# Optimization experiments

Hardware: AMD Instinct MI355X
Metric: run time of the kernel (lower is better)

Reference implementation:

```python
import jax, jax.numpy as jnp
import numpy as np

H = 8      # n_heads
DK = 64    # d_k per head
EPS = 1e-5       # InstanceNorm1d eps
SLOPE = 0.01     # LeakyReLU negative slope


def setup_inputs() -> dict:
    key = jax.random.key(0)
    ks = jax.random.split(key, 6)
    B, C, L = 16, 256, 1024
    HD = H * DK  # 512
    return {
        "x": jax.random.normal(ks[0], (B, C, L), dtype=jnp.float32),
        "Wq": jax.random.normal(ks[1], (HD, C), dtype=jnp.float32) * 0.02,
        "Wk": jax.random.normal(ks[2], (HD, C), dtype=jnp.float32) * 0.02,
        "Wv": jax.random.normal(ks[3], (HD, C), dtype=jnp.float32) * 0.02,
        "Wo": jax.random.normal(ks[4], (C, HD), dtype=jnp.float32) * 0.02,
        "gamma": jax.random.normal(ks[5], (1,), dtype=jnp.float32),
    }


def reference(x, Wq, Wk, Wv, Wo, gamma):
    B, C, L = x.shape
    # conv1x1 projections (bias=False) == channel matmuls -> [B, H*DK, L]
    # then reshape/permute into heads: [B, H, L, DK]
    def proj(W):
        y = jnp.einsum('oc,bcl->bol', W, x)          # [B, H*DK, L]
        return y.reshape(B, H, DK, L).transpose(0, 1, 3, 2)  # [B, H, L, DK]

    q, k, v = proj(Wq), proj(Wk), proj(Wv)
    # softmax-free linear attention: (Q K^T / d_k) V
    logits = jnp.einsum('bhld,bhmd->bhlm', q, k) / DK  # [B, H, L, L]
    out = jnp.einsum('bhlm,bhmd->bhld', logits, v)     # [B, H, L, DK]
    # merge heads back to channel-first [B, H*DK, L]
    merged = out.transpose(0, 1, 3, 2).reshape(B, H * DK, L)
    # output conv1x1 -> [B, C, L]
    o = jnp.einsum('oc,bcl->bol', Wo, merged)
    # InstanceNorm1d (affine=False): normalize over L per (b, c)
    mu = jnp.mean(o, axis=-1, keepdims=True)
    var = jnp.var(o, axis=-1, keepdims=True)
    o = (o - mu) * jax.lax.rsqrt(var + EPS)
    # gamma-scaled residual + LeakyReLU
    y = o * gamma + x
    return jnp.where(y >= 0, y, SLOPE * y)
```

## Files before the change

kernel.cpp:

```cpp
#include <hip/hip_runtime.h>

typedef __bf16 bf16;
typedef bf16 bf16x8 __attribute__((ext_vector_type(8)));
typedef bf16 bf16x4 __attribute__((ext_vector_type(4)));
typedef float f32x4 __attribute__((ext_vector_type(4)));

#define EPS 1e-5f
#define SLOPE 0.01f

__device__ __forceinline__ void gld_lds16(const bf16* g, bf16* l) {
    __builtin_amdgcn_global_load_lds(
        (const __attribute__((address_space(1))) unsigned int*)g,
        (__attribute__((address_space(3))) unsigned int*)l, 16, 0, 0);
}

__global__ __launch_bounds__(256) void prep_kernel(
    const float* __restrict__ x,
    const float* __restrict__ Wq, const float* __restrict__ Wk,
    const float* __restrict__ Wv, const float* __restrict__ Wo,
    bf16* __restrict__ xT, bf16* __restrict__ xB,
    bf16* __restrict__ WkB, bf16* __restrict__ WvB,
    bf16* __restrict__ WoB, bf16* __restrict__ WqT)
{
    __shared__ float tile[64][65];
    const int id = blockIdx.x;
    const int t = threadIdx.x;
    if (id < 1024) {
        const int lt = id & 15, ct = (id >> 4) & 3, b = id >> 6;
        {
            const int cl = t >> 2;
            const int l4 = (t & 3) << 4;
            const float* src = x + (size_t)(b * 256 + ct * 64 + cl) * 1024 + lt * 64 + l4;
            float4 v0 = ((const float4*)src)[0];
            float4 v1 = ((const float4*)src)[1];
            float4 v2 = ((const float4*)src)[2];
            float4 v3 = ((const float4*)src)[3];
            bf16x8 r0, r1;
            r0[0]=(bf16)v0.x; r0[1]=(bf16)v0.y; r0[2]=(bf16)v0.z; r0[3]=(bf16)v0.w;
            r0[4]=(bf16)v1.x; r0[5]=(bf16)v1.y; r0[6]=(bf16)v1.z; r0[7]=(bf16)v1.w;
            r1[0]=(bf16)v2.x; r1[1]=(bf16)v2.y; r1[2]=(bf16)v2.z; r1[3]=(bf16)v2.w;
            r1[4]=(bf16)v3.x; r1[5]=(bf16)v3.y; r1[6]=(bf16)v3.z; r1[7]=(bf16)v3.w;
            bf16* xbd = xB + (size_t)(b * 256 + ct * 64 + cl) * 1024 + lt * 64 + l4;
            *(bf16x8*)xbd = r0;
            *(bf16x8*)(xbd + 8) = r1;
            float* tr = &tile[cl][l4];
            tr[0]=v0.x; tr[1]=v0.y; tr[2]=v0.z; tr[3]=v0.w;
            tr[4]=v1.x; tr[5]=v1.y; tr[6]=v1.z; tr[7]=v1.w;
            tr[8]=v2.x; tr[9]=v2.y; tr[10]=v2.z; tr[11]=v2.w;
            tr[12]=v3.x; tr[13]=v3.y; tr[14]=v3.z; tr[15]=v3.w;
        }
        __syncthreads();
        {
            const int lw = t >> 2;
            const int ec = (t & 3) << 4;
            bf16x8 o0, o1;
            #pragma unroll
            for (int ii = 0; ii < 8; ++ii) {
                o0[ii] = (bf16)tile[ec + ii][lw];
                o1[ii] = (bf16)tile[ec + 8 + ii][lw];
            }
            bf16* dst = xT + (size_t)(b * 1024 + lt * 64 + lw) * 256 + ct * 64 + ec;
            *(bf16x8*)dst = o0;
            *(bf16x8*)(dst + 8) = o1;
        }
    } else if (id < 1408) {
        const int i = (id - 1024) * 1024 + t * 4;
        const float* src; bf16* dst;
        if (i < 131072)      { src = Wk + i;            dst = WkB + i; }
        else if (i < 262144) { src = Wv + (i - 131072); dst = WvB + (i - 131072); }
        else                 { src = Wo + (i - 262144); dst = WoB + (i - 262144); }
        float4 v = *(const float4*)src;
        bf16x4 o;
        o[0]=(bf16)v.x; o[1]=(bf16)v.y; o[2]=(bf16)v.z; o[3]=(bf16)v.w;
        *(bf16x4*)dst = o;
    } else {
        const int id2 = id - 1408;
        const int h = id2 >> 2, ct = id2 & 3;
        {
            const int e  = t >> 2;
            const int c4 = (t & 3) << 4;
            const float* src = Wq + (size_t)(h * 64 + e) * 256 + ct * 64 + c4;
            float4 v0 = ((const float4*)src)[0];
            float4 v1 = ((const float4*)src)[1];
            float4 v2 = ((const float4*)src)[2];
            float4 v3 = ((const float4*)src)[3];
            float* tr = &tile[e][c4];
            tr[0]=v0.x; tr[1]=v0.y; tr[2]=v0.z; tr[3]=v0.w;
            tr[4]=v1.x; tr[5]=v1.y; tr[6]=v1.z; tr[7]=v1.w;
            tr[8]=v2.x; tr[9]=v2.y; tr[10]=v2.z; tr[11]=v2.w;
            tr[12]=v3.x; tr[13]=v3.y; tr[14]=v3.z; tr[15]=v3.w;
        }
        __syncthreads();
        {
            const int c  = t >> 2;
            const int e4 = (t & 3) << 4;
            bf16x8 o0, o1;
            #pragma unroll
            for (int ii = 0; ii < 8; ++ii) {
                o0[ii] = (bf16)tile[e4 + ii][c];
                o1[ii] = (bf16)tile[e4 + 8 + ii][c];
            }
            bf16* dst = WqT + (size_t)h * 16384 + (size_t)(ct * 64 + c) * 64 + e4;
            *(bf16x8*)dst = o0;
            *(bf16x8*)(dst + 8) = o1;
        }
    }
}

template<int KDIM, typename OutT>
__global__ __launch_bounds__(256) void gemm128_bt(
    const bf16* __restrict__ A, const bf16* __restrict__ Bt, OutT* __restrict__ C,
    long long sA, long long sBt, long long sC, int ldC)
{
    __shared__ bf16 As[128 * 32];
    __shared__ bf16 Bs[128 * 32];
    const int z = blockIdx.z;
    A  += (size_t)z * sA;
    Bt += (size_t)z * sBt;
    C  += (size_t)z * sC;
    const int m0 = blockIdx.x * 128;
    const int n0 = blockIdx.y * 128;
    const int t = threadIdx.x, w = t >> 6, l = t & 63;
    const int srow = w * 16 + (l >> 2);
    const int ske  = (l & 3) * 8;
    const bf16* ga = A  + (size_t)(m0 + srow) * KDIM + ske;
    const bf16* gb = Bt + (size_t)(n0 + srow) * KDIM + ske;
    bf16* la = As + srow * 32 + ske;
    bf16* lb = Bs + srow * 32 + ske;
    const int lm = l & 15, lq = l >> 4;
    const int wm = (w & 1) * 64, wn = (w >> 1) * 64;

    f32x4 acc[4][4] = {};
    for (int kt = 0; kt < KDIM / 32; ++kt) {
        const int k0 = kt * 32;
        gld_lds16(ga + k0, la);
        gld_lds16(ga + k0 + (size_t)64 * KDIM, la + 64 * 32);
        gld_lds16(gb + k0, lb);
        gld_lds16(gb + k0 + (size_t)64 * KDIM, lb + 64 * 32);
        __syncthreads();
        bf16x8 af[4], bfr[4];
        #pragma unroll
        for (int i = 0; i < 4; ++i)
            af[i] = *(const bf16x8*)(As + (wm + i * 16 + lm) * 32 + lq * 8);
        #pragma unroll
        for (int j = 0; j < 4; ++j)
            bfr[j] = *(const bf16x8*)(Bs + (wn + j * 16 + lm) * 32 + lq * 8);
        #pragma unroll
        for (int i = 0; i < 4; ++i)
            #pragma unroll
            for (int j = 0; j < 4; ++j)
                acc[i][j] = __builtin_amdgcn_mfma_f32_16x16x32_bf16(af[i], bfr[j], acc[i][j], 0, 0, 0);
        __syncthreads();
    }
    #pragma unroll
    for (int i = 0; i < 4; ++i)
        #pragma unroll
        for (int j = 0; j < 4; ++j) {
            const int row = m0 + wm + i * 16 + lq * 4;
            const int col = n0 + wn + j * 16 + lm;
            OutT* cp = C + (size_t)row * ldC + col;
            #pragma unroll
            for (int r = 0; r < 4; ++r)
                cp[(size_t)r * ldC] = (OutT)acc[i][j][r];
        }
}

__global__ __launch_bounds__(256) void tm_kernel(
    const bf16* __restrict__ S, const bf16* __restrict__ WkB,
    const bf16* __restrict__ WqT, bf16* __restrict__ WmT)
{
    __shared__ __align__(16) bf16 regA[16384];
    __shared__ __align__(16) bf16 Qb[16384];
    bf16* Sc = regA;
    bf16* Kc = regA + 8192;
    bf16* Tb = regA;

    const int bh = blockIdx.x;
    const int b = bh >> 3, h = bh & 7;
    const bf16* Sg = S   + (size_t)b * 131072 + (size_t)h * 64 * 256;
    const bf16* Kg = WkB + (size_t)h * 64 * 256;
    const bf16* Qg = WqT + (size_t)h * 16384;
    const int t = threadIdx.x, w = t >> 6, l = t & 63;
    const int lm = l & 15, lq = l >> 4;

    #pragma unroll
    for (int it = 0; it < 8; ++it) {
        const int idx = it * 256 + t;
        const int r = idx >> 3, s = idx & 7;
        gld_lds16(Qg + (size_t)r * 64 + (s ^ (r & 7)) * 8, Qb + r * 64 + s * 8);
    }

    f32x4 accT[4] = {};
    for (int ck = 0; ck < 2; ++ck) {
        const int k0 = ck * 128;
        #pragma unroll
        for (int it = 0; it < 4; ++it) {
            const int idx = it * 256 + t;
            const int r = idx >> 4, s = idx & 15;
            const int gs = (s ^ (r & 7)) * 8;
            gld_lds16(Sg + (size_t)r * 256 + k0 + gs, Sc + r * 128 + s * 8);
            gld_lds16(Kg + (size_t)r * 256 + k0 + gs, Kc + r * 128 + s * 8);
        }
        __syncthreads();
        #pragma unroll
        for (int ks = 0; ks < 4; ++ks) {
            const int q = ks * 4 + lq;
            const int ra = w * 16 + lm;
            bf16x8 a = *(const bf16x8*)(Sc + ra * 128 + (q ^ (ra & 7)) * 8);
            #pragma unroll
            for (int nf = 0; nf < 4; ++nf) {
                const int rb = nf * 16 + lm;
                bf16x8 bb = *(const bf16x8*)(Kc + rb * 128 + (q ^ (rb & 7)) * 8);
                accT[nf] = __builtin_amdgcn_mfma_f32_16x16x32_bf16(a, bb, accT[nf], 0, 0, 0);
            }
        }
        __syncthreads();
    }
    #pragma unroll
    for (int nf = 0; nf < 4; ++nf)
        #pragma unroll
        for (int ri = 0; ri < 4; ++ri) {
            const int row = w * 16 + lq * 4 + ri;
            const int col = nf * 16 + lm;
            Tb[row * 64 + (((col >> 3) ^ (row & 7)) << 3) + (col & 7)] =
                (bf16)(accT[nf][ri] * 0.015625f);
        }
    __syncthreads();

    f32x4 accM[4][4] = {};
    #pragma unroll
    for (int ks = 0; ks < 2; ++ks) {
        const int q = ks * 4 + lq;
        bf16x8 bfrag[4];
        #pragma unroll
        for (int nf = 0; nf < 4; ++nf) {
            const int rb = nf * 16 + lm;
            bfrag[nf] = *(const bf16x8*)(Tb + rb * 64 + (q ^ (rb & 7)) * 8);
        }
        #pragma unroll
        for (int mf = 0; mf < 4; ++mf) {
            const int ra = w * 64 + mf * 16 + lm;
            bf16x8 a = *(const bf16x8*)(Qb + ra * 64 + (q ^ (ra & 7)) * 8);
            #pragma unroll
            for (int nf = 0; nf < 4; ++nf)
                accM[mf][nf] = __builtin_amdgcn_mfma_f32_16x16x32_bf16(a, bfrag[nf], accM[mf][nf], 0, 0, 0);
        }
    }
    bf16* Wg = WmT + (size_t)b * 131072 + h * 64;
    #pragma unroll
    for (int mf = 0; mf < 4; ++mf)
        #pragma unroll
        for (int nf = 0; nf < 4; ++nf)
            #pragma unroll
            for (int ri = 0; ri < 4; ++ri) {
                const int c = w * 64 + mf * 16 + lq * 4 + ri;
                const int d = nf * 16 + lm;
                Wg[(size_t)c * 512 + d] = (bf16)accM[mf][nf][ri];
            }
}

__global__ __launch_bounds__(256) void norm_kernel(
    const bf16* __restrict__ o, const bf16* __restrict__ xB,
    const float* __restrict__ gamma, float* __restrict__ y)
{
    const size_t row = blockIdx.x;
    const bf16* orow = o + row * 1024;
    const bf16* xrow = xB + row * 1024;
    float* yrow = y + row * 1024;
    const int tid = threadIdx.x;

    bf16x4 ov = *(const bf16x4*)(orow + tid * 4);
    float4 v = {(float)ov[0], (float)ov[1], (float)ov[2], (float)ov[3]};
    float s  = v.x + v.y + v.z + v.w;
    float ss = v.x * v.x + v.y * v.y + v.z * v.z + v.w * v.w;
    #pragma unroll
    for (int off = 32; off > 0; off >>= 1) {
        s  += __shfl_down(s, off);
        ss += __shfl_down(ss, off);
    }
    __shared__ float red[10];
    const int wave = tid >> 6, lane = tid & 63;
    if (lane == 0) { red[wave] = s; red[4 + wave] = ss; }
    __syncthreads();
    if (tid == 0) {
        float a  = red[0] + red[1] + red[2] + red[3];
        float b2 = red[4] + red[5] + red[6] + red[7];
        float mu = a * (1.0f / 1024.0f);
        float var = b2 * (1.0f / 1024.0f) - mu * mu;
        red[8] = mu;
        red[9] = rsqrtf(var + EPS);
    }
    __syncthreads();
    const float mu = red[8], inv = red[9], g = gamma[0];
    bf16x4 xv4 = *(const bf16x4*)(xrow + tid * 4);
    float4 r;
    r.x = (v.x - mu) * inv * g + (float)xv4[0];
    r.y = (v.y - mu) * inv * g + (float)xv4[1];
    r.z = (v.z - mu) * inv * g + (float)xv4[2];
    r.w = (v.w - mu) * inv * g + (float)xv4[3];
    r.x = r.x >= 0.f ? r.x : SLOPE * r.x;
    r.y = r.y >= 0.f ? r.y : SLOPE * r.y;
    r.z = r.z >= 0.f ? r.z : SLOPE * r.z;
    r.w = r.w >= 0.f ? r.w : SLOPE * r.w;
    ((float4*)yrow)[tid] = r;
}

extern "C" void kernel_launch(void* const* d_in, const int* in_sizes, int n_in,
                              void* d_out, int out_size, void* d_ws, size_t ws_size,
                              hipStream_t stream) {
    const float* x     = (const float*)d_in[0];
    const float* Wq    = (const float*)d_in[1];
    const float* Wk    = (const float*)d_in[2];
    const float* Wv    = (const float*)d_in[3];
    const float* Wo    = (const float*)d_in[4];
    const float* gamma = (const float*)d_in[5];
    float* y = (float*)d_out;

    char* wsb = (char*)d_ws;
    bf16* xT  = (bf16*)(wsb);
    bf16* xB  = (bf16*)(wsb +  8388608);
    bf16* WkB = (bf16*)(wsb + 16777216);
    bf16* WvB = (bf16*)(wsb + 17039360);
    bf16* WoB = (bf16*)(wsb + 17301504);
    bf16* WqT = (bf16*)(wsb + 17563648);
    bf16* G   = (bf16*)(wsb + 17825792);
    bf16* S   = (bf16*)(wsb + 19922944);
    bf16* WmT = (bf16*)(wsb + 24117248);
    bf16* Wt  = (bf16*)(wsb + 28311552);
    bf16* o   = (bf16*)(wsb + 30408704);

    prep_kernel<<<dim3(1440), 256, 0, stream>>>(x, Wq, Wk, Wv, Wo, xT, xB, WkB, WvB, WoB, WqT);

    gemm128_bt<1024, bf16><<<dim3(2, 2, 16), 256, 0, stream>>>(
        xB, xB, G, 262144LL, 262144LL, 65536LL, 256);

    gemm128_bt<256, bf16><<<dim3(4, 2, 16), 256, 0, stream>>>(
        WvB, G, S, 0LL, 65536LL, 131072LL, 256);

    tm_kernel<<<dim3(128), 256, 0, stream>>>(S, WkB, WqT, WmT);

    gemm128_bt<512, bf16><<<dim3(2, 2, 16), 256, 0, stream>>>(
        WoB, WmT, Wt, 0LL, 131072LL, 65536LL, 256);

    gemm128_bt<256, bf16><<<dim3(2, 8, 16), 256, 0, stream>>>(
        Wt, xT, o, 65536LL, 262144LL, 262144LL, 1024);

    norm_kernel<<<dim3(4096), 256, 0, stream>>>(o, xB, gamma, y);
}
```

Measured before the change: 139.0 us.

## Fuse projection chain into one kernel and fuse output GEMMs with instance norm

Merges the S = Wv·G GEMM into the per-head tm kernel, so S stays in LDS and is never written to or read back from global memory. Separately, it fuses the Wo·WmT GEMM, the final GEMM against x and the InstanceNorm/residual/LeakyReLU epilogue into one kernel per (batch, 16-channel tile). This removes the Wt and o intermediates and cuts the launch count from seven to four. The trade-off is fewer, heavier blocks (128 and 256) with large LDS footprints, which may underfill the GPU. The Wt product is also recomputed per channel tile rather than shared.

```diff
diff --git a/kernel.cpp b/kernel.cpp
--- a/kernel.cpp
+++ b/kernel.cpp
@@ -165,85 +165,151 @@
         }
 }
 
-__global__ __launch_bounds__(256) void tm_kernel(
-    const bf16* __restrict__ S, const bf16* __restrict__ WkB,
-    const bf16* __restrict__ WqT, bf16* __restrict__ WmT)
+__global__ __launch_bounds__(256) void chain_kernel(
+    const bf16* __restrict__ G, const bf16* __restrict__ WvB,
+    const bf16* __restrict__ WkB, const bf16* __restrict__ WqT,
+    bf16* __restrict__ WmT)
 {
-    __shared__ __align__(16) bf16 regA[16384];
-    __shared__ __align__(16) bf16 Qb[16384];
-    bf16* Sc = regA;
-    bf16* Kc = regA + 8192;
-    bf16* Tb = regA;
+    __shared__ __align__(16) bf16 bufA[64 * 256];
+    __shared__ __align__(16) bf16 bufB[256 * 64];
+    __shared__ __align__(16) bf16 Ss[64 * 256];
+    __shared__ __align__(16) bf16 Tb[64 * 64];
 
     const int bh = blockIdx.x;
     const int b = bh >> 3, h = bh & 7;
-    const bf16* Sg = S   + (size_t)b * 131072 + (size_t)h * 64 * 256;
-    const bf16* Kg = WkB + (size_t)h * 64 * 256;
-    const bf16* Qg = WqT + (size_t)h * 16384;
     const int t = threadIdx.x, w = t >> 6, l = t & 63;
     const int lm = l & 15, lq = l >> 4;
 
     #pragma unroll
     for (int it = 0; it < 8; ++it) {
-        const int idx = it * 256 + t;
-        const int r = idx >> 3, s = idx & 7;
-        gld_lds16(Qg + (size_t)r * 64 + (s ^ (r & 7)) * 8, Qb + r * 64 + s * 8);
-    }
-
-    f32x4 accT[4] = {};
-    for (int ck = 0; ck < 2; ++ck) {
-        const int k0 = ck * 128;
-        #pragma unroll
-        for (int it = 0; it < 4; ++it) {
-            const int idx = it * 256 + t;
-            const int r = idx >> 4, s = idx & 15;
-            const int gs = (s ^ (r & 7)) * 8;
-            gld_lds16(Sg + (size_t)r * 256 + k0 + gs, Sc + r * 128 + s * 8);
-            gld_lds16(Kg + (size_t)r * 256 + k0 + gs, Kc + r * 128 + s * 8);
-        }
-        __syncthreads();
-        #pragma unroll
-        for (int ks = 0; ks < 4; ++ks) {
-            const int q = ks * 4 + lq;
-            const int ra = w * 16 + lm;
-            bf16x8 a = *(const bf16x8*)(Sc + ra * 128 + (q ^ (ra & 7)) * 8);
+        const int slot = it * 256 + t;
+        const int d = slot >> 5, seg = slot & 31;
+        const int kq = (seg & 24) | ((seg & 7) ^ (d & 7));
+        gld_lds16(WvB + (size_t)(h * 64 + d) * 256 + kq * 8, bufA + slot * 8);
+    }
+    f32x4 accS[4][4] = {};
+    for (int ck = 0; ck < 4; ++ck) {
+        #pragma unroll
+        for (int it = 0; it < 8; ++it) {
+            const int slot = it * 256 + t;
+            const int cp = slot >> 3, seg = slot & 7;
+            const int kq = seg ^ (cp & 7);
+            gld_lds16(G + (size_t)b * 65536 + (size_t)cp * 256 + ck * 64 + kq * 8,
+                      bufB + slot * 8);
+        }
+        __syncthreads();
+        #pragma unroll
+        for (int kt = 0; kt < 2; ++kt) {
+            bf16x8 af[4], bfr[4];
+            #pragma unroll
+            for (int mf = 0; mf < 4; ++mf) {
+                const int m = mf * 16 + lm;
+                const int kqg = ck * 8 + kt * 4 + lq;
+                const int seg = (kqg & 24) | ((kqg & 7) ^ (m & 7));
+                af[mf] = *(const bf16x8*)(bufA + m * 256 + seg * 8);
+            }
             #pragma unroll
             for (int nf = 0; nf < 4; ++nf) {
-                const int rb = nf * 16 + lm;
-                bf16x8 bb = *(const bf16x8*)(Kc + rb * 128 + (q ^ (rb & 7)) * 8);
-                accT[nf] = __builtin_amdgcn_mfma_f32_16x16x32_bf16(a, bb, accT[nf], 0, 0, 0);
-            }
-        }
-        __syncthreads();
-    }
-    #pragma unroll
-    for (int nf = 0; nf < 4; ++nf)
-        #pragma unroll
-        for (int ri = 0; ri < 4; ++ri) {
-            const int row = w * 16 + lq * 4 + ri;
-            const int col = nf * 16 + lm;
-            Tb[row * 64 + (((col >> 3) ^ (row & 7)) << 3) + (col & 7)] =
-                (bf16)(accT[nf][ri] * 0.015625f);
-        }
+                const int n = w * 64 + nf * 16 + lm;
+                const int kq = kt * 4 + lq;
+                const int seg = kq ^ (n & 7);
+                bfr[nf] = *(const bf16x8*)(bufB + n * 64 + seg * 8);
+            }
+            #pragma unroll
+            for (int mf = 0; mf < 4; ++mf)
+                #pragma unroll
+                for (int nf = 0; nf < 4; ++nf)
+                    accS[mf][nf] = __builtin_amdgcn_mfma_f32_16x16x32_bf16(
+                        af[mf], bfr[nf], accS[mf][nf], 0, 0, 0);
+        }
+        __syncthreads();
+    }
+    #pragma unroll
+    for (int mf = 0; mf < 4; ++mf)
+        #pragma unroll
+        for (int nf = 0; nf < 4; ++nf)
+            #pragma unroll
+            for (int r = 0; r < 4; ++r) {
+                const int d = mf * 16 + lq * 4 + r;
+                const int cp = w * 64 + nf * 16 + lm;
+                const int s32 = cp >> 3;
+                const int s = (s32 & 24) | ((s32 & 7) ^ (d & 7));
+                Ss[d * 256 + s * 8 + (cp & 7)] = (bf16)accS[mf][nf][r];
+            }
+    #pragma unroll
+    for (int it = 0; it < 8; ++it) {
+        const int slot = it * 256 + t;
+        const int e = slot >> 5, seg = slot & 31;
+        const int kq = (seg & 24) | ((seg & 7) ^ (e & 7));
+        gld_lds16(WkB + (size_t)(h * 64 + e) * 256 + kq * 8, bufB + slot * 8);
+    }
     __syncthreads();
 
+    const int mh = (w & 1) * 32, nh = (w >> 1) * 32;
+    f32x4 accT[2][2] = {};
+    #pragma unroll
+    for (int kt = 0; kt < 8; ++kt) {
+        bf16x8 af[2], bfr[2];
+        #pragma unroll
+        for (int mf = 0; mf < 2; ++mf) {
+            const int m = mh + mf * 16 + lm;
+            const int kqg = kt * 4 + lq;
+            const int seg = (kqg & 24) | ((kqg & 7) ^ (m & 7));
+            af[mf] = *(const bf16x8*)(Ss + m * 256 + seg * 8);
+        }
+        #pragma unroll
+        for (int nf = 0; nf < 2; ++nf) {
+            const int n = nh + nf * 16 + lm;
+            const int kqg = kt * 4 + lq;
+            const int seg = (kqg & 24) | ((kqg & 7) ^ (n & 7));
+            bfr[nf] = *(const bf16x8*)(bufB + n * 256 + seg * 8);
+        }
+        #pragma unroll
+        for (int mf = 0; mf < 2; ++mf)
+            #pragma unroll
+            for (int nf = 0; nf < 2; ++nf)
+                accT[mf][nf] = __builtin_amdgcn_mfma_f32_16x16x32_bf16(
+                    af[mf], bfr[nf], accT[mf][nf], 0, 0, 0);
+    }
+    __syncthreads();
+    #pragma unroll
+    for (int mf = 0; mf < 2; ++mf)
+        #pragma unroll
+        for (int nf = 0; nf < 2; ++nf)
+            #pragma unroll
+            for (int r = 0; r < 4; ++r) {
+                const int d = mh + mf * 16 + lq * 4 + r;
+                const int e = nh + nf * 16 + lm;
+                const int seg = (e >> 3) ^ (d & 7);
+                Tb[d * 64 + seg * 8 + (e & 7)] = (bf16)(accT[mf][nf][r] * 0.015625f);
+            }
+    #pragma unroll
+    for (int it = 0; it < 8; ++it) {
+        const int slot = it * 256 + t;
+        const int c = slot >> 3, seg = slot & 7;
+        const int kq = seg ^ (c & 7);
+        gld_lds16(WqT + (size_t)h * 16384 + (size_t)c * 64 + kq * 8, bufA + slot * 8);
+    }
+    __syncthreads();
+
     f32x4 accM[4][4] = {};
     #pragma unroll
-    for (int ks = 0; ks < 2; ++ks) {
-        const int q = ks * 4 + lq;
-        bf16x8 bfrag[4];
+    for (int kt = 0; kt < 2; ++kt) {
+        const int kq = kt * 4 + lq;
+        bf16x8 bfr[4];
         #pragma unroll
         for (int nf = 0; nf < 4; ++nf) {
-            const int rb = nf * 16 + lm;
-            bfrag[nf] = *(const bf16x8*)(Tb + rb * 64 + (q ^ (rb & 7)) * 8);
+            const int n = nf * 16 + lm;
+            bfr[nf] = *(const bf16x8*)(Tb + n * 64 + (kq ^ (n & 7)) * 8);
         }
         #pragma unroll
         for (int mf = 0; mf < 4; ++mf) {
-            const int ra = w * 64 + mf * 16 + lm;
-            bf16x8 a = *(const bf16x8*)(Qb + ra * 64 + (q ^ (ra & 7)) * 8);
+            const int m = w * 64 + mf * 16 + lm;
+            bf16x8 a = *(const bf16x8*)(bufA + m * 64 + (kq ^ (m & 7)) * 8);
             #pragma unroll
             for (int nf = 0; nf < 4; ++nf)
-                accM[mf][nf] = __builtin_amdgcn_mfma_f32_16x16x32_bf16(a, bfrag[nf], accM[mf][nf], 0, 0, 0);
+                accM[mf][nf] = __builtin_amdgcn_mfma_f32_16x16x32_bf16(
+                    a, bfr[nf], accM[mf][nf], 0, 0, 0);
         }
     }
     bf16* Wg = WmT + (size_t)b * 131072 + h * 64;
@@ -252,57 +318,163 @@
         #pragma unroll
         for (int nf = 0; nf < 4; ++nf)
             #pragma unroll
-            for (int ri = 0; ri < 4; ++ri) {
-                const int c = w * 64 + mf * 16 + lq * 4 + ri;
+            for (int r = 0; r < 4; ++r) {
+                const int c = w * 64 + mf * 16 + lq * 4 + r;
                 const int d = nf * 16 + lm;
-                Wg[(size_t)c * 512 + d] = (bf16)accM[mf][nf][ri];
+                Wg[(size_t)c * 512 + d] = (bf16)accM[mf][nf][r];
             }
 }
 
-__global__ __launch_bounds__(256) void norm_kernel(
-    const bf16* __restrict__ o, const bf16* __restrict__ xB,
+__global__ __launch_bounds__(256) void outnorm_kernel(
+    const bf16* __restrict__ WoB, const bf16* __restrict__ WmT,
+    const bf16* __restrict__ xT, const bf16* __restrict__ xB,
     const float* __restrict__ gamma, float* __restrict__ y)
 {
-    const size_t row = blockIdx.x;
-    const bf16* orow = o + row * 1024;
-    const bf16* xrow = xB + row * 1024;
-    float* yrow = y + row * 1024;
-    const int tid = threadIdx.x;
-
-    bf16x4 ov = *(const bf16x4*)(orow + tid * 4);
-    float4 v = {(float)ov[0], (float)ov[1], (float)ov[2], (float)ov[3]};
-    float s  = v.x + v.y + v.z + v.w;
-    float ss = v.x * v.x + v.y * v.y + v.z * v.z + v.w * v.w;
-    #pragma unroll
-    for (int off = 32; off > 0; off >>= 1) {
-        s  += __shfl_down(s, off);
-        ss += __shfl_down(ss, off);
-    }
-    __shared__ float red[10];
-    const int wave = tid >> 6, lane = tid & 63;
-    if (lane == 0) { red[wave] = s; red[4 + wave] = ss; }
+    __shared__ __align__(16) bf16 chunkBuf[32768];
+    __shared__ __align__(16) bf16 WoS[16 * 512];
+    __shared__ __align__(16) bf16 WtS[16 * 256];
+    __shared__ float redS[4][16], redQ[4][16], bmu[16], binv[16];
+
+    const int b = blockIdx.x >> 4, ct = blockIdx.x & 15;
+    const int c0 = ct * 16;
+    const int t = threadIdx.x, w = t >> 6, l = t & 63;
+    const int lm = l & 15, lq = l >> 4;
+
+    #pragma unroll
+    for (int it = 0; it < 4; ++it) {
+        const int slot = it * 256 + t;
+        const int co = slot >> 6, seg = slot & 63;
+        const int kq = (seg & 56) | ((seg & 7) ^ (co & 7));
+        gld_lds16(WoB + (size_t)(c0 + co) * 512 + kq * 8, WoS + slot * 8);
+    }
+    f32x4 acc1[4] = {};
+    for (int ck = 0; ck < 8; ++ck) {
+        const int k0 = ck * 64;
+        #pragma unroll
+        for (int it = 0; it < 8; ++it) {
+            const int slot = it * 256 + t;
+            const int ci = slot >> 3, seg = slot & 7;
+            const int kq = seg ^ (ci & 7);
+            gld_lds16(WmT + (size_t)b * 131072 + (size_t)ci * 512 + k0 + kq * 8,
+                      chunkBuf + slot * 8);
+        }
+        __syncthreads();
+        #pragma unroll
+        for (int kt = 0; kt < 2; ++kt) {
+            const int kqg = ck * 8 + kt * 4 + lq;
+            const int sa = (kqg & 56) | ((kqg & 7) ^ (lm & 7));
+            bf16x8 a = *(const bf16x8*)(WoS + lm * 512 + sa * 8);
+            #pragma unroll
+            for (int nf = 0; nf < 4; ++nf) {
+                const int n = w * 64 + nf * 16 + lm;
+                const int kq = kt * 4 + lq;
+                bf16x8 bb = *(const bf16x8*)(chunkBuf + n * 64 + (kq ^ (n & 7)) * 8);
+                acc1[nf] = __builtin_amdgcn_mfma_f32_16x16x32_bf16(a, bb, acc1[nf], 0, 0, 0);
+            }
+        }
+        __syncthreads();
+    }
+    #pragma unroll
+    for (int nf = 0; nf < 4; ++nf)
+        #pragma unroll
+        for (int r = 0; r < 4; ++r) {
+            const int co = lq * 4 + r;
+            const int ci = w * 64 + nf * 16 + lm;
+            const int s32 = ci >> 3;
+            const int s = (s32 & 24) | ((s32 & 7) ^ (co & 7));
+            WtS[co * 256 + s * 8 + (ci & 7)] = (bf16)acc1[nf][r];
+        }
     __syncthreads();
-    if (tid == 0) {
-        float a  = red[0] + red[1] + red[2] + red[3];
-        float b2 = red[4] + red[5] + red[6] + red[7];
-        float mu = a * (1.0f / 1024.0f);
-        float var = b2 * (1.0f / 1024.0f) - mu * mu;
-        red[8] = mu;
-        red[9] = rsqrtf(var + EPS);
-    }
+
+    f32x4 acc2[16] = {};
+    for (int ck = 0; ck < 8; ++ck) {
+        const int k0 = ck * 32;
+        #pragma unroll
+        for (int it = 0; it < 16; ++it) {
+            const int slot = it * 256 + t;
+            const int ln = slot >> 2, seg = slot & 3;
+            const int kq = seg ^ (ln & 3);
+            gld_lds16(xT + (size_t)b * 262144 + (size_t)ln * 256 + k0 + kq * 8,
+                      chunkBuf + slot * 8);
+        }
+        __syncthreads();
+        const int kqg = ck * 4 + lq;
+        const int sa = (kqg & 24) | ((kqg & 7) ^ (lm & 7));
+        bf16x8 a = *(const bf16x8*)(WtS + lm * 256 + sa * 8);
+        #pragma unroll
+        for (int j = 0; j < 16; ++j) {
+            const int n = w * 256 + j * 16 + lm;
+            bf16x8 bb = *(const bf16x8*)(chunkBuf + n * 32 + ((lq ^ (n & 3)) * 8));
+            acc2[j] = __builtin_amdgcn_mfma_f32_16x16x32_bf16(a, bb, acc2[j], 0, 0, 0);
+        }
+        __syncthreads();
+    }
+
+    float s[4] = {}, q[4] = {};
+    #pragma unroll
+    for (int j = 0; j < 16; ++j)
+        #pragma unroll
+        for (int r = 0; r < 4; ++r) {
+            const float v = acc2[j][r];
+            s[r] += v; q[r] += v * v;
+        }
+    #pragma unroll
+    for (int off = 1; off < 16; off <<= 1)
+        #pragma unroll
+        for (int r = 0; r < 4; ++r) {
+            s[r] += __shfl_xor(s[r], off);
+            q[r] += __shfl_xor(q[r], off);
+        }
+    if (lm == 0)
+        #pragma unroll
+        for (int r = 0; r < 4; ++r) {
+            redS[w][lq * 4 + r] = s[r];
+            redQ[w][lq * 4 + r] = q[r];
+        }
     __syncthreads();
-    const float mu = red[8], inv = red[9], g = gamma[0];
-    bf16x4 xv4 = *(const bf16x4*)(xrow + tid * 4);
-    float4 r;
-    r.x = (v.x - mu) * inv * g + (float)xv4[0];
-    r.y = (v.y - mu) * inv * g + (float)xv4[1];
-    r.z = (v.z - mu) * inv * g + (float)xv4[2];
-    r.w = (v.w - mu) * inv * g + (float)xv4[3];
-    r.x = r.x >= 0.f ? r.x : SLOPE * r.x;
-    r.y = r.y >= 0.f ? r.y : SLOPE * r.y;
-    r.z = r.z >= 0.f ? r.z : SLOPE * r.z;
-    r.w = r.w >= 0.f ? r.w : SLOPE * r.w;
-    ((float4*)yrow)[tid] = r;
+    if (t < 16) {
+        float S = redS[0][t] + redS[1][t] + redS[2][t] + redS[3][t];
+        float Q = redQ[0][t] + redQ[1][t] + redQ[2][t] + redQ[3][t];
+        const float mu = S * (1.0f / 1024.0f);
+        const float var = Q * (1.0f / 1024.0f) - mu * mu;
+        bmu[t] = mu;
+        binv[t] = rsqrtf(var + EPS);
+    }
+    bf16* otile = chunkBuf;
+    #pragma unroll
+    for (int j = 0; j < 16; ++j)
+        #pragma unroll
+        for (int r = 0; r < 4; ++r)
+            otile[(lq * 4 + r) * 1032 + w * 256 + j * 16 + lm] = (bf16)acc2[j][r];
+    __syncthreads();
+
+    const float g = gamma[0];
+    const int qd = t >> 6, l64 = t & 63;
+    #pragma unroll
+    for (int i = 0; i < 4; ++i) {
+        const int c = qd * 4 + i;
+        const float mu = bmu[c], inv = binv[c];
+        bf16x8 o0 = *(const bf16x8*)(otile + c * 1032 + l64 * 16);
+        bf16x8 o1 = *(const bf16x8*)(otile + c * 1032 + l64 * 16 + 8);
+        const bf16* xr = xB + (size_t)(b * 256 + c0 + c) * 1024 + l64 * 16;
+        bf16x8 x0 = *(const bf16x8*)xr;
+        bf16x8 x1 = *(const bf16x8*)(xr + 8);
+        float* yp = y + (size_t)(b * 256 + c0 + c) * 1024 + l64 * 16;
+        float4 out[4];
+        #pragma unroll
+        for (int kk = 0; kk < 8; ++kk) {
+            float v0 = ((float)o0[kk] - mu) * inv * g + (float)x0[kk];
+            float v1 = ((float)o1[kk] - mu) * inv * g + (float)x1[kk];
+            v0 = v0 >= 0.f ? v0 : SLOPE * v0;
+            v1 = v1 >= 0.f ? v1 : SLOPE * v1;
+            ((float*)out)[kk] = v0;
+            ((float*)out)[8 + kk] = v1;
+        }
+        ((float4*)yp)[0] = out[0];
+        ((float4*)yp)[1] = out[1];
+        ((float4*)yp)[2] = out[2];
+        ((float4*)yp)[3] = out[3];
+    }
 }
 
 extern "C" void kernel_launch(void* const* d_in, const int* in_sizes, int n_in,
@@ -324,26 +496,14 @@
     bf16* WoB = (bf16*)(wsb + 17301504);
     bf16* WqT = (bf16*)(wsb + 17563648);
     bf16* G   = (bf16*)(wsb + 17825792);
-    bf16* S   = (bf16*)(wsb + 19922944);
-    bf16* WmT = (bf16*)(wsb + 24117248);
-    bf16* Wt  = (bf16*)(wsb + 28311552);
-    bf16* o   = (bf16*)(wsb + 30408704);
+    bf16* WmT = (bf16*)(wsb + 19922944);
 
     prep_kernel<<<dim3(1440), 256, 0, stream>>>(x, Wq, Wk, Wv, Wo, xT, xB, WkB, WvB, WoB, WqT);
 
     gemm128_bt<1024, bf16><<<dim3(2, 2, 16), 256, 0, stream>>>(
         xB, xB, G, 262144LL, 262144LL, 65536LL, 256);
 
-    gemm128_bt<256, bf16><<<dim3(4, 2, 16), 256, 0, stream>>>(
-        WvB, G, S, 0LL, 65536LL, 131072LL, 256);
-
-    tm_kernel<<<dim3(128), 256, 0, stream>>>(S, WkB, WqT, WmT);
-
-    gemm128_bt<512, bf16><<<dim3(2, 2, 16), 256, 0, stream>>>(
-        WoB, WmT, Wt, 0LL, 131072LL, 65536LL, 256);
-
-    gemm128_bt<256, bf16><<<dim3(2, 8, 16), 256, 0, stream>>>(
-        Wt, xT, o, 65536LL, 262144LL, 262144LL, 1024);
-
-    norm_kernel<<<dim3(4096), 256, 0, stream>>>(o, xB, gamma, y);
+    chain_kernel<<<dim3(128), 256, 0, stream>>>(G, WvB, WkB, WqT, WmT);
+
+    outnorm_kernel<<<dim3(256), 256, 0, stream>>>(WoB, WmT, xT, xB, gamma, y);
 }
```

New measurement: 140.2 us (median of 2 runs). No clear change (+0.8%).
